# Performance work log

Hardware: AMD Instinct MI355X
Metric: run time of the kernel (lower is better)

The kernel has to match this reference:

```python
import jax, jax.numpy as jnp
import numpy as np

N_NODES = 100000


def _mean_aggregate(feat, src, dst, num_nodes):
    # mean over edges (src -> dst) of feat[src], grouped by dst; 0 for isolated nodes
    summed = jax.ops.segment_sum(feat[src], dst, num_segments=num_nodes)  # [N, d]
    deg = jax.ops.segment_sum(jnp.ones((src.shape[0],), feat.dtype), dst,
                              num_segments=num_nodes)  # [N]
    return summed / jnp.maximum(deg, 1.0)[:, None]


def setup_inputs() -> dict:
    key = jax.random.key(0)
    k1, k2, k3 = jax.random.split(key, 3)
    feat = jax.random.normal(k1, (N_NODES, 128), dtype=jnp.float32)
    # fc_self_neigh weight: Linear(3*in_feats=384 -> out_feats=128), no bias
    W = jax.random.normal(k2, (128, 384), dtype=jnp.float32) * 0.05
    edge_index = jax.random.randint(k3, (2, 800000), 0, N_NODES, dtype=jnp.int32)
    return {"feat": feat, "W": W, "edge_index": edge_index}


def reference(feat, W, edge_index):
    src, dst = edge_index[0], edge_index[1]
    n = feat.shape[0]
    h_self = feat  # feat_drop = 0.0
    # forward SAGE: mean of in-neighbor (source) features per destination node
    fwd_neigh = _mean_aggregate(feat, src, dst, n)
    # backward SAGE on reversed graph: mean of out-neighbor (dest) features per source node
    bwd_neigh = _mean_aggregate(feat, dst, src, n)
    h = jnp.concatenate((h_self, fwd_neigh, bwd_neigh), axis=1)  # [N, 3*d]
    rst = h @ W.T  # [N, out_feats], bias=False
    return jax.nn.relu(rst)
```

## Files before the change

kernel.cpp:

```cpp
#include <hip/hip_runtime.h>
#include <hip/hip_bf16.h>

#define D 128
#define CHUNK 1024
#define NXCD 8

typedef __attribute__((ext_vector_type(8))) short bf16x8;
typedef __attribute__((ext_vector_type(4))) float f32x4;

__device__ inline float bflo(unsigned u) { return __uint_as_float(u << 16); }
__device__ inline float bfhi(unsigned u) { return __uint_as_float(u & 0xffff0000u); }
__device__ inline unsigned short f2bf(float f) {
    __hip_bfloat16 h = __float2bfloat16(f);
    return *reinterpret_cast<unsigned short*>(&h);
}
__device__ inline unsigned pack2bf(float lo, float hi) {
    return (unsigned)f2bf(lo) | ((unsigned)f2bf(hi) << 16);
}

__global__ __launch_bounds__(256) void convert_kernel(
    const float* __restrict__ feat, unsigned short* __restrict__ featb, int n4f,
    const float* __restrict__ W, unsigned short* __restrict__ Wb, int n4w,
    int* __restrict__ cnt, int n2)
{
    int i = blockIdx.x * blockDim.x + threadIdx.x;
    const int stride = gridDim.x * blockDim.x;
    const int n4 = n4f + n4w;
    for (int j = i; j < n4; j += stride) {
        const float* x; unsigned short* y; int k;
        if (j < n4f) { x = feat; y = featb; k = j; }
        else         { x = W;    y = Wb;    k = j - n4f; }
        float4 v = *reinterpret_cast<const float4*>(&x[(size_t)k * 4]);
        uint2 o;
        o.x = pack2bf(v.x, v.y);
        o.y = pack2bf(v.z, v.w);
        *reinterpret_cast<uint2*>(&y[(size_t)k * 4]) = o;
    }
    for (int z = i; z < n2; z += stride) cnt[z] = 0;
}

__global__ __launch_bounds__(256) void hist_rank_kernel(
    const int* __restrict__ src, const int* __restrict__ dst,
    int* __restrict__ cnt, int* __restrict__ rankF, int* __restrict__ rankB,
    int E, int N)
{
    const int e = blockIdx.x * blockDim.x + threadIdx.x;
    if (e < E) {
        rankF[e] = atomicAdd(&cnt[dst[e]], 1);
        rankB[e] = atomicAdd(&cnt[N + src[e]], 1);
    }
}

__global__ __launch_bounds__(256) void scan1_kernel(
    const int* __restrict__ cnt, int* __restrict__ blk, int n2)
{
    __shared__ int red[256];
    const int b = blockIdx.x, t = threadIdx.x;
    const int base = b * CHUNK + t * 4;
    int s = 0;
    if (base + 3 < n2) {
        int4 v = *reinterpret_cast<const int4*>(&cnt[base]);
        s = v.x + v.y + v.z + v.w;
    } else {
        for (int j = 0; j < 4; ++j) { int idx = base + j; if (idx < n2) s += cnt[idx]; }
    }
    red[t] = s; __syncthreads();
    for (int o = 128; o > 0; o >>= 1) { if (t < o) red[t] += red[t + o]; __syncthreads(); }
    if (t == 0) blk[b] = red[0];
}

__global__ __launch_bounds__(256) void scan3_kernel(
    const int* __restrict__ cnt, const int* __restrict__ blk,
    int* __restrict__ off, int n2, int total, int NB)
{
    __shared__ int sh[256];
    __shared__ int bs[256];
    const int b = blockIdx.x, t = threadIdx.x;

    bs[t] = (t < NB) ? blk[t] : 0;
    __syncthreads();
    for (int o = 1; o < 256; o <<= 1) {
        int v = (t >= o) ? bs[t - o] : 0;
        __syncthreads();
        bs[t] += v;
        __syncthreads();
    }
    const int blkpref = (b > 0) ? bs[b - 1] : 0;

    const int base = b * CHUNK + t * 4;
    int v[4]; int s = 0;
    for (int j = 0; j < 4; ++j) { int idx = base + j; v[j] = (idx < n2) ? cnt[idx] : 0; s += v[j]; }
    sh[t] = s; __syncthreads();
    for (int o = 1; o < 256; o <<= 1) {
        int x = (t >= o) ? sh[t - o] : 0;
        __syncthreads();
        sh[t] += x;
        __syncthreads();
    }
    int excl = blkpref + ((t > 0) ? sh[t - 1] : 0);
    for (int j = 0; j < 4; ++j) {
        int idx = base + j;
        if (idx < n2) off[idx] = excl;
        excl += v[j];
    }
    if (b == 0 && t == 0) off[n2] = total;
}

__global__ __launch_bounds__(256) void scatter_ids_kernel(
    const int* __restrict__ src, const int* __restrict__ dst,
    const int* __restrict__ off,
    const int* __restrict__ rankF, const int* __restrict__ rankB,
    int* __restrict__ csr, int E, int N, int npr)
{
    const int grp = blockIdx.x & (NXCD - 1);
    const int bIn = blockIdx.x >> 3;
    const int nbk = gridDim.x >> 3;
    const int lo = grp * npr;
    const int hi = lo + npr;

    int i = bIn * 256 + threadIdx.x;
    const int stride = nbk * 256;
    for (int e = i; e < E; e += stride) {
        const int s = src[e];
        const int d = dst[e];
        if (d >= lo && d < hi) {
            csr[off[d] + rankF[e]] = s;
        }
        if (s >= lo && s < hi) {
            csr[off[N + s] + rankB[e]] = d;
        }
    }
}

__global__ __launch_bounds__(256) void gather_mean_kernel(
    const unsigned short* __restrict__ featb, const int* __restrict__ off,
    const int* __restrict__ csr, unsigned short* __restrict__ meanb, int n2)
{
    const int tid = blockIdx.x * 256 + threadIdx.x;
    const int seg = tid >> 4;
    const int l = tid & 15;
    if (seg >= n2) return;

    const int beg = off[seg], end = off[seg + 1];
    float a0=0,a1=0,a2=0,a3=0,a4=0,a5=0,a6=0,a7=0;

    int e = beg;
    for (; e + 3 < end; e += 4) {
        const int n0 = __builtin_nontemporal_load(&csr[e]);
        const int n1 = __builtin_nontemporal_load(&csr[e + 1]);
        const int n2i = __builtin_nontemporal_load(&csr[e + 2]);
        const int n3 = __builtin_nontemporal_load(&csr[e + 3]);
        const uint4 v0 = *reinterpret_cast<const uint4*>(featb + (size_t)n0 * D + l * 8);
        const uint4 v1 = *reinterpret_cast<const uint4*>(featb + (size_t)n1 * D + l * 8);
        const uint4 v2 = *reinterpret_cast<const uint4*>(featb + (size_t)n2i * D + l * 8);
        const uint4 v3 = *reinterpret_cast<const uint4*>(featb + (size_t)n3 * D + l * 8);
        a0 += (bflo(v0.x) + bflo(v1.x)) + (bflo(v2.x) + bflo(v3.x));
        a1 += (bfhi(v0.x) + bfhi(v1.x)) + (bfhi(v2.x) + bfhi(v3.x));
        a2 += (bflo(v0.y) + bflo(v1.y)) + (bflo(v2.y) + bflo(v3.y));
        a3 += (bfhi(v0.y) + bfhi(v1.y)) + (bfhi(v2.y) + bfhi(v3.y));
        a4 += (bflo(v0.z) + bflo(v1.z)) + (bflo(v2.z) + bflo(v3.z));
        a5 += (bfhi(v0.z) + bfhi(v1.z)) + (bfhi(v2.z) + bfhi(v3.z));
        a6 += (bflo(v0.w) + bflo(v1.w)) + (bflo(v2.w) + bflo(v3.w));
        a7 += (bfhi(v0.w) + bfhi(v1.w)) + (bfhi(v2.w) + bfhi(v3.w));
    }
    for (; e < end; ++e) {
        const int n0 = __builtin_nontemporal_load(&csr[e]);
        const uint4 v0 = *reinterpret_cast<const uint4*>(featb + (size_t)n0 * D + l * 8);
        a0 += bflo(v0.x); a1 += bfhi(v0.x);
        a2 += bflo(v0.y); a3 += bfhi(v0.y);
        a4 += bflo(v0.z); a5 += bfhi(v0.z);
        a6 += bflo(v0.w); a7 += bfhi(v0.w);
    }

    const int deg = end - beg;
    const float inv = 1.0f / (float)((deg > 1) ? deg : 1);
    uint4 o;
    o.x = pack2bf(a0 * inv, a1 * inv);
    o.y = pack2bf(a2 * inv, a3 * inv);
    o.z = pack2bf(a4 * inv, a5 * inv);
    o.w = pack2bf(a6 * inv, a7 * inv);
    *reinterpret_cast<uint4*>(meanb + (size_t)seg * D + l * 8) = o;
}

__global__ __launch_bounds__(512) void mfma_gemm_kernel(
    const unsigned short* __restrict__ featb,
    const unsigned short* __restrict__ meanb,
    const unsigned short* __restrict__ Wb,
    float* __restrict__ out, int N)
{
    __shared__ unsigned short wlds[2][128 * 128];

    const int t = threadIdx.x;
    const int wv = t >> 6;
    const int lane = t & 63;
    const int r = lane & 15;
    const int q = lane >> 4;

    const int row0 = blockIdx.x * 128 + wv * 16;
    const int row = row0 + r;
    const int rowc = (row < N) ? row : (N - 1);

    const unsigned short* h0 = featb + (size_t)rowc * D;
    const unsigned short* h1 = meanb + (size_t)rowc * D;
    const unsigned short* h2 = meanb + ((size_t)N + rowc) * D;
    bf16x8 af[12];
#pragma unroll
    for (int kk = 0; kk < 4; ++kk) {
        af[kk]     = *reinterpret_cast<const bf16x8*>(h0 + kk * 32 + q * 8);
        af[4 + kk] = *reinterpret_cast<const bf16x8*>(h1 + kk * 32 + q * 8);
        af[8 + kk] = *reinterpret_cast<const bf16x8*>(h2 + kk * 32 + q * 8);
    }

    const int sc = t >> 2;
    const int sq = t & 3;
    const char* wsrc = reinterpret_cast<const char*>(Wb) + (size_t)sc * 768;
    const int swz = (sc & 7) << 4;

    f32x4 acc[8];
#pragma unroll
    for (int n = 0; n < 8; ++n) acc[n] = (f32x4){0.f, 0.f, 0.f, 0.f};

    {
        uint4 st[4];
#pragma unroll
        for (int j = 0; j < 4; ++j)
            st[j] = *reinterpret_cast<const uint4*>(wsrc + j * 64 + sq * 16);
        char* wb0 = reinterpret_cast<char*>(&wlds[0][0]) + sc * 256;
#pragma unroll
        for (int j = 0; j < 4; ++j)
            *reinterpret_cast<uint4*>(wb0 + ((j * 64 + sq * 16) ^ swz)) = st[j];
    }
    __syncthreads();

#pragma unroll
    for (int ci = 0; ci < 3; ++ci) {
        uint4 nx[4];
        if (ci < 2) {
#pragma unroll
            for (int j = 0; j < 4; ++j)
                nx[j] = *reinterpret_cast<const uint4*>(
                    wsrc + (ci + 1) * 256 + j * 64 + sq * 16);
        }

        const char* wl = reinterpret_cast<const char*>(&wlds[ci & 1][0]);
#pragma unroll
        for (int kk = 0; kk < 4; ++kk) {
            const bf16x8 bh = af[ci * 4 + kk];
#pragma unroll
            for (int n = 0; n < 8; ++n) {
                const int c = n * 16 + r;
                const bf16x8 aw = *reinterpret_cast<const bf16x8*>(
                    wl + c * 256 + ((kk * 64 + q * 16) ^ ((c & 7) << 4)));
                acc[n] = __builtin_amdgcn_mfma_f32_16x16x32_bf16(aw, bh, acc[n], 0, 0, 0);
            }
        }

        if (ci < 2) {
            char* wbn = reinterpret_cast<char*>(&wlds[(ci + 1) & 1][0]) + sc * 256;
#pragma unroll
            for (int j = 0; j < 4; ++j)
                *reinterpret_cast<uint4*>(wbn + ((j * 64 + sq * 16) ^ swz)) = nx[j];
            __syncthreads();
        }
    }

    if (row < N) {
        float* orow = out + (size_t)row * D;
#pragma unroll
        for (int n = 0; n < 8; ++n) {
            float4 v;
            v.x = fmaxf(acc[n][0], 0.0f);
            v.y = fmaxf(acc[n][1], 0.0f);
            v.z = fmaxf(acc[n][2], 0.0f);
            v.w = fmaxf(acc[n][3], 0.0f);
            *reinterpret_cast<float4*>(orow + n * 16 + q * 4) = v;
        }
    }
}

extern "C" void kernel_launch(void* const* d_in, const int* in_sizes, int n_in,
                              void* d_out, int out_size, void* d_ws, size_t ws_size,
                              hipStream_t stream) {
    const float* feat = (const float*)d_in[0];
    const float* W    = (const float*)d_in[1];
    const int*   ei   = (const int*)d_in[2];
    float*       out  = (float*)d_out;

    const int E = in_sizes[2] / 2;
    const int N = in_sizes[0] / D;
    const int n2 = 2 * N;
    const int* src = ei;
    const int* dst = ei + E;

    int* cnt   = (int*)d_ws;
    int* off   = cnt + n2;
    int* blk   = off + (n2 + 4);
    int* rankF = blk + 256;
    int* rankB = rankF + E;
    int* csr   = rankB + E;
    unsigned short* featb = (unsigned short*)(csr + 2 * E);
    unsigned short* Wb    = featb + (size_t)N * D;
    unsigned short* meanb = Wb + 128 * 384;

    const int NB = (n2 + CHUNK - 1) / CHUNK;
    const int npr = (N + NXCD - 1) / NXCD;
    const int n4f = N * D / 4;
    const int n4w = 128 * 384 / 4;

    convert_kernel<<<2048, 256, 0, stream>>>(feat, featb, n4f, W, Wb, n4w,
                                             cnt, n2);
    hist_rank_kernel<<<(E + 255) / 256, 256, 0, stream>>>(src, dst, cnt,
                                                          rankF, rankB, E, N);

    scan1_kernel<<<NB, 256, 0, stream>>>(cnt, blk, n2);
    scan3_kernel<<<NB, 256, 0, stream>>>(cnt, blk, off, n2, 2 * E, NB);
    scatter_ids_kernel<<<2048, 256, 0, stream>>>(src, dst, off, rankF, rankB,
                                                 csr, E, N, npr);

    const int gather_blocks = (n2 * 16 + 255) / 256;
    gather_mean_kernel<<<gather_blocks, 256, 0, stream>>>(featb, off, csr, meanb, n2);

    mfma_gemm_kernel<<<(N + 127) / 128, 512, 0, stream>>>(featb, meanb, Wb, out, N);
}
```

Before: 226.5 us.

## Fuse bf16 convert and histogram kernels into one launch, memset counts separately

```diff
diff --git a/kernel.cpp b/kernel.cpp
--- a/kernel.cpp
+++ b/kernel.cpp
@@ -18,36 +18,34 @@
     return (unsigned)f2bf(lo) | ((unsigned)f2bf(hi) << 16);
 }
 
-__global__ __launch_bounds__(256) void convert_kernel(
+__global__ __launch_bounds__(256) void convert_hist_kernel(
     const float* __restrict__ feat, unsigned short* __restrict__ featb, int n4f,
     const float* __restrict__ W, unsigned short* __restrict__ Wb, int n4w,
-    int* __restrict__ cnt, int n2)
-{
-    int i = blockIdx.x * blockDim.x + threadIdx.x;
-    const int stride = gridDim.x * blockDim.x;
-    const int n4 = n4f + n4w;
-    for (int j = i; j < n4; j += stride) {
-        const float* x; unsigned short* y; int k;
-        if (j < n4f) { x = feat; y = featb; k = j; }
-        else         { x = W;    y = Wb;    k = j - n4f; }
-        float4 v = *reinterpret_cast<const float4*>(&x[(size_t)k * 4]);
-        uint2 o;
-        o.x = pack2bf(v.x, v.y);
-        o.y = pack2bf(v.z, v.w);
-        *reinterpret_cast<uint2*>(&y[(size_t)k * 4]) = o;
-    }
-    for (int z = i; z < n2; z += stride) cnt[z] = 0;
-}
-
-__global__ __launch_bounds__(256) void hist_rank_kernel(
     const int* __restrict__ src, const int* __restrict__ dst,
     int* __restrict__ cnt, int* __restrict__ rankF, int* __restrict__ rankB,
-    int E, int N)
-{
-    const int e = blockIdx.x * blockDim.x + threadIdx.x;
-    if (e < E) {
-        rankF[e] = atomicAdd(&cnt[dst[e]], 1);
-        rankB[e] = atomicAdd(&cnt[N + src[e]], 1);
+    int E, int N, int ncb)
+{
+    if ((int)blockIdx.x < ncb) {
+        int i = blockIdx.x * 256 + threadIdx.x;
+        const int stride = ncb * 256;
+        const int n4 = n4f + n4w;
+        for (int j = i; j < n4; j += stride) {
+            const float* x; unsigned short* y; int k;
+            if (j < n4f) { x = feat; y = featb; k = j; }
+            else         { x = W;    y = Wb;    k = j - n4f; }
+            float4 v = *reinterpret_cast<const float4*>(&x[(size_t)k * 4]);
+            uint2 o;
+            o.x = pack2bf(v.x, v.y);
+            o.y = pack2bf(v.z, v.w);
+            *reinterpret_cast<uint2*>(&y[(size_t)k * 4]) = o;
+        }
+    } else {
+        int i = (blockIdx.x - ncb) * 256 + threadIdx.x;
+        const int stride = (gridDim.x - ncb) * 256;
+        for (int e = i; e < E; e += stride) {
+            rankF[e] = atomicAdd(&cnt[dst[e]], 1);
+            rankB[e] = atomicAdd(&cnt[N + src[e]], 1);
+        }
     }
 }
 
@@ -146,10 +144,7 @@
 
     int e = beg;
     for (; e + 3 < end; e += 4) {
-        const int n0 = __builtin_nontemporal_load(&csr[e]);
-        const int n1 = __builtin_nontemporal_load(&csr[e + 1]);
-        const int n2i = __builtin_nontemporal_load(&csr[e + 2]);
-        const int n3 = __builtin_nontemporal_load(&csr[e + 3]);
+        const int n0 = csr[e], n1 = csr[e + 1], n2i = csr[e + 2], n3 = csr[e + 3];
         const uint4 v0 = *reinterpret_cast<const uint4*>(featb + (size_t)n0 * D + l * 8);
         const uint4 v1 = *reinterpret_cast<const uint4*>(featb + (size_t)n1 * D + l * 8);
         const uint4 v2 = *reinterpret_cast<const uint4*>(featb + (size_t)n2i * D + l * 8);
@@ -164,7 +159,7 @@
         a7 += (bfhi(v0.w) + bfhi(v1.w)) + (bfhi(v2.w) + bfhi(v3.w));
     }
     for (; e < end; ++e) {
-        const int n0 = __builtin_nontemporal_load(&csr[e]);
+        const int n0 = csr[e];
         const uint4 v0 = *reinterpret_cast<const uint4*>(featb + (size_t)n0 * D + l * 8);
         a0 += bflo(v0.x); a1 += bfhi(v0.x);
         a2 += bflo(v0.y); a3 += bfhi(v0.y);
@@ -306,11 +301,12 @@
     const int npr = (N + NXCD - 1) / NXCD;
     const int n4f = N * D / 4;
     const int n4w = 128 * 384 / 4;
-
-    convert_kernel<<<2048, 256, 0, stream>>>(feat, featb, n4f, W, Wb, n4w,
-                                             cnt, n2);
-    hist_rank_kernel<<<(E + 255) / 256, 256, 0, stream>>>(src, dst, cnt,
-                                                          rankF, rankB, E, N);
+    const int ncb = 2048;
+
+    hipMemsetAsync(cnt, 0, (size_t)n2 * sizeof(int), stream);
+
+    convert_hist_kernel<<<ncb + 2048, 256, 0, stream>>>(
+        feat, featb, n4f, W, Wb, n4w, src, dst, cnt, rankF, rankB, E, N, ncb);
 
     scan1_kernel<<<NB, 256, 0, stream>>>(cnt, blk, n2);
     scan3_kernel<<<NB, 256, 0, stream>>>(cnt, blk, off, n2, 2 * E, NB);
```

Result: no change. 227.3 us (+0.4%).
